# Performance work log

Measured on AMD Instinct MI355X. Metric: run time of the kernel, lower is better.

Reference implementation:

```python
import jax, jax.numpy as jnp
import numpy as np

B, T, I, H, O = 64, 512, 256, 512, 10


def _init(key, shape, fan):
    k = 1.0 / np.sqrt(fan)
    return jax.random.uniform(key, shape, jnp.float32, -k, k)


def setup_inputs() -> dict:
    key = jax.random.key(0)
    ks = jax.random.split(key, 16)
    return {
        "x": jax.random.normal(ks[0], (B, T, I), jnp.float32),
        # LSTM params (PyTorch gate order: i, f, g, o)
        "lstm_w_ih": _init(ks[1], (4 * H, I), H),
        "lstm_w_hh": _init(ks[2], (4 * H, H), H),
        "lstm_b_ih": _init(ks[3], (4 * H,), H),
        "lstm_b_hh": _init(ks[4], (4 * H,), H),
        # GRU params (gate order: r, z, n)
        "gru_w_ih": _init(ks[5], (3 * H, H), H),
        "gru_w_hh": _init(ks[6], (3 * H, H), H),
        "gru_b_ih": _init(ks[7], (3 * H,), H),
        "gru_b_hh": _init(ks[8], (3 * H,), H),
        # RNN-tanh params
        "rnn_w_ih": _init(ks[9], (H, H), H),
        "rnn_w_hh": _init(ks[10], (H, H), H),
        "rnn_b_ih": _init(ks[11], (H,), H),
        "rnn_b_hh": _init(ks[12], (H,), H),
        # FC head
        "fc_w": _init(ks[13], (O, H), H),
        "fc_b": _init(ks[14], (O,), H),
    }


def _lstm(x, w_ih, w_hh, b_ih, b_hh):
    # Precompute input projections for all timesteps: [T, B, 4H]
    xg = (jnp.einsum('bti,gi->btg', x, w_ih) + b_ih + b_hh).transpose(1, 0, 2)
    h0 = jnp.zeros((x.shape[0], w_hh.shape[1]), x.dtype)

    def step(carry, xt):
        h, c = carry
        g = xt + h @ w_hh.T
        i, f, gg, o = jnp.split(g, 4, axis=-1)
        c = jax.nn.sigmoid(f) * c + jax.nn.sigmoid(i) * jnp.tanh(gg)
        h = jax.nn.sigmoid(o) * jnp.tanh(c)
        return (h, c), h

    _, hs = jax.lax.scan(step, (h0, h0), xg)
    return hs.transpose(1, 0, 2)  # [B, T, H]


def _gru(x, w_ih, w_hh, b_ih, b_hh):
    xg = (jnp.einsum('bti,gi->btg', x, w_ih) + b_ih).transpose(1, 0, 2)  # [T,B,3H]
    h0 = jnp.zeros((x.shape[0], w_hh.shape[1]), x.dtype)

    def step(h, xt):
        hg = h @ w_hh.T + b_hh
        xr, xz, xn = jnp.split(xt, 3, axis=-1)
        hr, hz, hn = jnp.split(hg, 3, axis=-1)
        r = jax.nn.sigmoid(xr + hr)
        z = jax.nn.sigmoid(xz + hz)
        n = jnp.tanh(xn + r * hn)
        h = (1.0 - z) * n + z * h
        return h, h

    _, hs = jax.lax.scan(step, h0, xg)
    return hs.transpose(1, 0, 2)


def _rnn_tanh(x, w_ih, w_hh, b_ih, b_hh):
    xg = (jnp.einsum('bti,gi->btg', x, w_ih) + b_ih + b_hh).transpose(1, 0, 2)
    h0 = jnp.zeros((x.shape[0], w_hh.shape[1]), x.dtype)

    def step(h, xt):
        h = jnp.tanh(xt + h @ w_hh.T)
        return h, h

    _, hs = jax.lax.scan(step, h0, xg)
    return hs.transpose(1, 0, 2)


def reference(x, lstm_w_ih, lstm_w_hh, lstm_b_ih, lstm_b_hh,
              gru_w_ih, gru_w_hh, gru_b_ih, gru_b_hh,
              rnn_w_ih, rnn_w_hh, rnn_b_ih, rnn_b_hh,
              fc_w, fc_b):
    h = _lstm(x, lstm_w_ih, lstm_w_hh, lstm_b_ih, lstm_b_hh)
    h = _gru(h, gru_w_ih, gru_w_hh, gru_b_ih, gru_b_hh)
    h = _rnn_tanh(h, rnn_w_ih, rnn_w_hh, rnn_b_ih, rnn_b_hh)
    last = h[:, -1]  # [B, H]
    return last @ fc_w.T + fc_b  # [B, O]
```

## Files before the change

### kernel.cpp

```cpp
#include <hip/hip_runtime.h>
#include <cstdint>

typedef _Float16 f16;
typedef _Float16 f16x8 __attribute__((ext_vector_type(8)));
typedef float f32x4 __attribute__((ext_vector_type(4)));
typedef unsigned u32;
typedef u32 u32x4 __attribute__((ext_vector_type(4)));

#define DI static __device__ __forceinline__

constexpr int T = 512, H = 512, Osz = 10;
constexpr int NWG = 256, NTH = 768;
constexpr int GW = 32;
constexpr int GB = 8;
constexpr int BH = 64 * H;
constexpr size_t XH_OFF = 512 * 1024;
constexpr int XH_GRP = 8 * T * 256;

DI float sigf(float x)   { return 1.f / (1.f + __expf(-x)); }
DI float tanhf_(float x) { return 1.f - 2.f / (__expf(2.f * x) + 1.f); }

DI f16x8 cvt8(const float* p) {
  f16x8 r;
#pragma unroll
  for (int j = 0; j < 8; ++j) r[j] = (f16)p[j];
  return r;
}

DI void pin8(f16x8& v) { asm volatile("" : "+v"(v)); }
DI u32 umin_(u32 a, u32 b) { return a < b ? a : b; }

DI void st16_sc1(void* p, f16 v) {
  asm volatile("global_store_short %0, %1, off sc1" :: "v"(p), "v"(v));
}
DI void st32_sc1(void* p, u32 v) {
  asm volatile("global_store_dword %0, %1, off sc1" :: "v"(p), "v"(v));
}
DI void st128_sc1(void* p, f16x8 v) {
  asm volatile("global_store_dwordx4 %0, %1, off sc1" :: "v"(p), "v"(v));
}
DI void vm_drain() { asm volatile("s_waitcnt vmcnt(0)" ::: "memory"); }

DI void ld2_sc1(const void* p0, const void* p1, f16x8& a, f16x8& b) {
  asm volatile(
    "global_load_dwordx4 %0, %2, off sc1\n\t"
    "global_load_dwordx4 %1, %3, off sc1\n\t"
    "s_waitcnt vmcnt(0)"
    : "=&v"(a), "=&v"(b)
    : "v"(p0), "v"(p1)
    : "memory");
}
DI void ld3_sc1(const void* p0, const void* p1, const void* p2,
                f16x8& a, f16x8& b, f16x8& c) {
  asm volatile(
    "global_load_dwordx4 %0, %3, off sc1\n\t"
    "global_load_dwordx4 %1, %4, off sc1\n\t"
    "global_load_dwordx4 %2, %5, off sc1\n\t"
    "s_waitcnt vmcnt(0)"
    : "=&v"(a), "=&v"(b), "=&v"(c)
    : "v"(p0), "v"(p1), "v"(p2)
    : "memory");
}

DI void ldrow8(const f16* base, f16x8* A) {
  asm volatile(
    "global_load_dwordx4 %0, %8, off sc1\n\t"
    "global_load_dwordx4 %1, %8, off offset:16 sc1\n\t"
    "global_load_dwordx4 %2, %8, off offset:32 sc1\n\t"
    "global_load_dwordx4 %3, %8, off offset:48 sc1\n\t"
    "global_load_dwordx4 %4, %8, off offset:64 sc1\n\t"
    "global_load_dwordx4 %5, %8, off offset:80 sc1\n\t"
    "global_load_dwordx4 %6, %8, off offset:96 sc1\n\t"
    "global_load_dwordx4 %7, %8, off offset:112 sc1\n\t"
    "s_waitcnt vmcnt(0)"
    : "=&v"(A[0]), "=&v"(A[1]), "=&v"(A[2]), "=&v"(A[3]),
      "=&v"(A[4]), "=&v"(A[5]), "=&v"(A[6]), "=&v"(A[7])
    : "v"(base)
    : "memory");
}

DI u32 slots_min(const u32* base) {
  u32x4 a0, a1, a2, a3, a4, a5, a6, a7;
  asm volatile(
    "global_load_dwordx4 %0, %8, off sc1\n\t"
    "global_load_dwordx4 %1, %8, off offset:16 sc1\n\t"
    "global_load_dwordx4 %2, %8, off offset:32 sc1\n\t"
    "global_load_dwordx4 %3, %8, off offset:48 sc1\n\t"
    "global_load_dwordx4 %4, %8, off offset:64 sc1\n\t"
    "global_load_dwordx4 %5, %8, off offset:80 sc1\n\t"
    "global_load_dwordx4 %6, %8, off offset:96 sc1\n\t"
    "global_load_dwordx4 %7, %8, off offset:112 sc1\n\t"
    "s_waitcnt vmcnt(0)"
    : "=&v"(a0), "=&v"(a1), "=&v"(a2), "=&v"(a3),
      "=&v"(a4), "=&v"(a5), "=&v"(a6), "=&v"(a7)
    : "v"(base)
    : "memory");
  u32 m = 0xFFFFFFFFu;
#define MIN4_(v) m = umin_(m, umin_(umin_(v[0], v[1]), umin_(v[2], v[3])))
  MIN4_(a0); MIN4_(a1); MIN4_(a2); MIN4_(a3);
  MIN4_(a4); MIN4_(a5); MIN4_(a6); MIN4_(a7);
#undef MIN4_
  return m;
}

DI void barrier_arrive(u32* slots, int w32, u32 val, int tid) {
  __syncthreads();
  if (tid == 0) st32_sc1(&slots[w32], val);
}
DI void barrier_wait(u32* slots, u32 target, int tid) {
  if (tid == 0) {
    u32 spins = 0;
    while (slots_min(slots) < target) {
      if (++spins > 300000u) break;
    }
  }
  __syncthreads();
}

__global__ __launch_bounds__(NTH, 1) void rnn_all(
    const float* __restrict__ x,
    const float* __restrict__ lwih, const float* __restrict__ lwhh,
    const float* __restrict__ lbih, const float* __restrict__ lbhh,
    const float* __restrict__ gwih, const float* __restrict__ gwhh,
    const float* __restrict__ gbih, const float* __restrict__ gbhh,
    const float* __restrict__ rwih, const float* __restrict__ rwhh,
    const float* __restrict__ rbih, const float* __restrict__ rbhh,
    const float* __restrict__ fcw, const float* __restrict__ fcb,
    float* __restrict__ out, char* __restrict__ ws)
{
  __shared__ __align__(16) u32 HSu[3 * 2048];
  __shared__ __align__(16) u32 XS[1024];
  __shared__ float P[12][16][20];
  __shared__ float sb[16][11];

  const int tid  = threadIdx.x;
  const int bid  = blockIdx.x;
  const int grp  = bid & 7;
  const int w32  = bid >> 3;
  const int bg0  = grp * GB;
  const int col0 = w32 * 16;
  const int w    = tid >> 6;
  const int lane = tid & 63;
  const int ln   = lane & 15;
  const int lk   = lane >> 4;

  u32* slots = reinterpret_cast<u32*>(ws) + (size_t)grp * 64;
  f16* HB = reinterpret_cast<f16*>(ws + 4096);
  f16* xh = reinterpret_cast<f16*>(ws + XH_OFF) + (size_t)grp * XH_GRP;

  f16x8 Bw[24];
#pragma unroll
  for (int ks = 16; ks < 24; ++ks) Bw[ks] = (f16x8)(f16)0.f;
  if (w < 4) {
    const int row = w * 512 + col0 + ln;
    const float* ph  = lwhh + (size_t)row * 512 + lk * 8;
    const float* px2 = lwih + (size_t)row * 256 + lk * 8;
#pragma unroll
    for (int ks = 0; ks < 16; ++ks) Bw[ks] = cvt8(ph + ks * 32);
#pragma unroll
    for (int ks = 0; ks < 8;  ++ks) Bw[16 + ks] = cvt8(px2 + ks * 32);
  } else if (w < 7) {
    const int row = (w - 4) * 512 + col0 + ln;
    const float* p = gwih + (size_t)row * 512 + lk * 8;
#pragma unroll
    for (int ks = 0; ks < 16; ++ks) Bw[ks] = cvt8(p + ks * 32);
  } else if (w < 10) {
    const int row = (w - 7) * 512 + col0 + ln;
    const float* p = gwhh + (size_t)row * 512 + lk * 8;
#pragma unroll
    for (int ks = 0; ks < 16; ++ks) Bw[ks] = cvt8(p + ks * 32);
  } else if (w == 10) {
    const float* p = rwhh + (size_t)(col0 + ln) * 512 + lk * 8;
#pragma unroll
    for (int ks = 0; ks < 16; ++ks) Bw[ks] = cvt8(p + ks * 32);
  } else {
    const float* p = rwih + (size_t)(col0 + ln) * 512 + lk * 8;
#pragma unroll
    for (int ks = 0; ks < 16; ++ks) Bw[ks] = cvt8(p + ks * 32);
  }
#pragma unroll
  for (int ks = 0; ks < 24; ++ks) pin8(Bw[ks]);

  for (int i = tid; i < 16 * 11; i += NTH) {
    int c = i / 11, j = i % 11, col = col0 + c;
    float v;
    if (j < 4)       v = lbih[j * 512 + col] + lbhh[j * 512 + col];
    else if (j < 7)  v = gbih[(j - 4) * 512 + col];
    else if (j < 10) v = gbhh[(j - 7) * 512 + col];
    else             v = rbih[col] + rbhh[col];
    sb[c][j] = v;
  }

  {
    const float* xg_ = x + (size_t)bg0 * (T * 256);
    for (int c = w32 * NTH + tid; c < XH_GRP / 8; c += GW * NTH) {
      const float* p = xg_ + (size_t)c * 8;
      f16x8 v;
#pragma unroll
      for (int j = 0; j < 8; ++j) v[j] = (f16)p[j];
      st128_sc1((void*)(xh + (size_t)c * 8), v);
    }
  }
  {
    int i = w32 * NTH + tid;
    if (i < 12288) {
      int buf = i >> 12, r = i & 4095, par = r >> 11, row = (r >> 8) & 7, cu = r & 255;
      void* p = (void*)(HB + (size_t)buf * 2 * BH + (size_t)par * BH
                           + (size_t)(bg0 + row) * H + cu * 2);
      st32_sc1(p, 0u);
    }
  }
  vm_drain();

  barrier_arrive(slots, w32, 1u, tid);

  float creg = 0.f, hgreg = 0.f;

  const int hbuf = (w < 7) ? 0 : ((w == 10) ? 2 : 1);

#pragma unroll 1
  for (int s = 0; s <= T + 1; ++s) {
    barrier_wait(slots, (u32)(s + 1), tid);

    const int cur = s & 1, prev = cur ^ 1;
    const int sc = (s < T) ? s : (T - 1);

    {
      int s0 = tid, s1 = tid + NTH;
      int b0 = s0 >> 9, r0 = s0 & 511, row0 = r0 >> 6, sr0 = r0 & 63;
      int b1 = s1 >> 9, r1 = s1 & 511, row1 = r1 >> 6, sr1 = r1 & 63;
      const f16* p0 = HB + (size_t)b0 * 2 * BH + (size_t)prev * BH
                         + (size_t)(bg0 + row0) * H + sr0 * 8;
      const f16* p1 = HB + (size_t)b1 * 2 * BH + (size_t)prev * BH
                         + (size_t)(bg0 + row1) * H + sr1 * 8;
      f16x8 va, vb;
      if (w < 4) {
        int xrow = tid >> 5, xsr = tid & 31;
        const f16* p2 = xh + ((size_t)xrow << 17) + (size_t)sc * 256 + xsr * 8;
        f16x8 vc;
        ld3_sc1(p0, p1, p2, va, vb, vc);
        *reinterpret_cast<f16x8*>(
            &XS[(((u32)xrow << 5) | ((u32)(xsr ^ xrow))) << 2]) = vc;
      } else {
        ld2_sc1(p0, p1, va, vb);
      }
      *reinterpret_cast<f16x8*>(&HSu[(b0 << 11) + row0 * 256 + ((sr0 ^ row0) << 2)]) = va;
      *reinterpret_cast<f16x8*>(&HSu[(b1 << 11) + row1 * 256 + ((sr1 ^ row1) << 2)]) = vb;
    }
    __syncthreads();

    const u32 rw_ = (u32)(ln & 7);
    const u32 abase = (u32)hbuf * 2048u + rw_ * 256u;

    f32x4 acc = {0.f, 0.f, 0.f, 0.f};
    if (w < 4) {
#pragma unroll
      for (int ks = 0; ks < 8; ++ks) {
        const f16x8 a = *reinterpret_cast<const f16x8*>(
            &XS[(((rw_ << 5) | (((u32)(ks * 4 + lk)) ^ rw_)) << 2)]);
        acc = __builtin_amdgcn_mfma_f32_16x16x32_f16(a, Bw[16 + ks], acc, 0, 0, 0);
      }
    }
#pragma unroll
    for (int ks = 0; ks < 16; ++ks) {
      const f16x8 a = *reinterpret_cast<const f16x8*>(
          &HSu[abase + ((((u32)(ks * 4 + lk)) ^ rw_) << 2)]);
      acc = __builtin_amdgcn_mfma_f32_16x16x32_f16(a, Bw[ks], acc, 0, 0, 0);
    }

    if (lk < 2)
      *reinterpret_cast<f32x4*>(&P[w][ln][lk * 4]) = acc;
    __syncthreads();

    if (tid < 128) {
      const int cb = tid >> 4, cc = tid & 15;
      const int gb = bg0 + cb, col = col0 + cc;

      float iL = sigf(P[0][cc][cb] + sb[cc][0]);
      float fL = sigf(P[1][cc][cb] + sb[cc][1]);
      float gL = tanhf_(P[2][cc][cb] + sb[cc][2]);
      float oL = sigf(P[3][cc][cb] + sb[cc][3]);
      float cn = fL * creg + iL * gL;
      float hLv = oL * tanhf_(cn);
      float xr = P[4][cc][cb] + sb[cc][4];
      float xz = P[5][cc][cb] + sb[cc][5];
      float xn = P[6][cc][cb] + sb[cc][6];
      float hr = P[7][cc][cb] + sb[cc][7];
      float hz = P[8][cc][cb] + sb[cc][8];
      float hn = P[9][cc][cb] + sb[cc][9];
      float rg = sigf(xr + hr), zg = sigf(xz + hz);
      float ng = tanhf_(xn + rg * hn);
      float hGv = (1.f - zg) * ng + zg * hgreg;
      float hRv = tanhf_(P[10][cc][cb] + P[11][cc][cb] + sb[cc][10]);

      f16* rowp = HB + (size_t)cur * BH + (size_t)gb * H + col;
      if (s < T)            { creg = cn; st16_sc1((void*)rowp, (f16)hLv); }
      if (s >= 1 && s <= T) { hgreg = hGv; st16_sc1((void*)(rowp + 2 * BH), (f16)hGv); }
      if (s >= 2)           st16_sc1((void*)(rowp + 4 * BH), (f16)hRv);
      vm_drain();
    }
    barrier_arrive(slots, w32, (u32)(s + 2), tid);
  }

  if (w32 == 0) {
    barrier_wait(slots, (u32)(T + 3), tid);
    if (tid < 640) {
      const f16* hlast = HB + 4 * BH + BH;
      int bo = tid >> 3, kq = tid & 7;
      int bl = bo / 10, o = bo % 10;
      const f16* ph = hlast + (size_t)(bg0 + bl) * H + kq * 64;
      const float* pw = fcw + (size_t)o * H + kq * 64;
      f16x8 v[8];
      ldrow8(ph, v);
      float a = 0.f;
#pragma unroll
      for (int q = 0; q < 8; ++q)
#pragma unroll
        for (int j = 0; j < 8; ++j) a += (float)v[q][j] * pw[q * 8 + j];
      a += __shfl_xor(a, 1);
      a += __shfl_xor(a, 2);
      a += __shfl_xor(a, 4);
      if (kq == 0) out[(bg0 + bl) * Osz + o] = a + fcb[o];
    }
  }
}

extern "C" void kernel_launch(void* const* d_in, const int* in_sizes, int n_in,
                              void* d_out, int out_size, void* d_ws, size_t ws_size,
                              hipStream_t stream) {
  (void)in_sizes; (void)n_in; (void)out_size; (void)ws_size;
  const float* x    = (const float*)d_in[0];
  const float* lwih = (const float*)d_in[1];
  const float* lwhh = (const float*)d_in[2];
  const float* lbih = (const float*)d_in[3];
  const float* lbhh = (const float*)d_in[4];
  const float* gwih = (const float*)d_in[5];
  const float* gwhh = (const float*)d_in[6];
  const float* gbih = (const float*)d_in[7];
  const float* gbhh = (const float*)d_in[8];
  const float* rwih = (const float*)d_in[9];
  const float* rwhh = (const float*)d_in[10];
  const float* rbih = (const float*)d_in[11];
  const float* rbhh = (const float*)d_in[12];
  const float* fcw  = (const float*)d_in[13];
  const float* fcb  = (const float*)d_in[14];
  float* outp = (float*)d_out;
  char* wsp   = (char*)d_ws;

  hipMemsetAsync(d_ws, 0, 4096, stream);

  rnn_all<<<dim3(NWG), dim3(NTH), 0, stream>>>(
      x, lwih, lwhh, lbih, lbhh, gwih, gwhh, gbih, gbhh,
      rwih, rwhh, rbih, rbhh, fcw, fcb, outp, wsp);
}
```

Measured before the change: 2.075 ms.

## Shrink per-step epilogue to one wave and drop the arrive barrier

The per-timestep gate epilogue now runs on a single 64-lane wave. Each lane computes two adjacent columns and writes them as packed 32-bit stores instead of 16-bit ones. That wave signals its own arrival right after draining its stores, so the block-wide __syncthreads before each arrive is gone. Spin-polling moves to a thread in another wave, and the loop-invariant load and LDS addresses are hoisted out of the step loop. The aim is to cut per-step sync and store latency on the serial critical path, at the cost of more ALU work per epilogue lane.

```diff
diff --git a/kernel.cpp b/kernel.cpp
--- a/kernel.cpp
+++ b/kernel.cpp
@@ -17,6 +17,8 @@
 constexpr size_t XH_OFF = 512 * 1024;
 constexpr int XH_GRP = 8 * T * 256;
 
+union F16x2 { u32 u; f16 h[2]; };
+
 DI float sigf(float x)   { return 1.f / (1.f + __expf(-x)); }
 DI float tanhf_(float x) { return 1.f - 2.f / (__expf(2.f * x) + 1.f); }
 
@@ -30,9 +32,6 @@
 DI void pin8(f16x8& v) { asm volatile("" : "+v"(v)); }
 DI u32 umin_(u32 a, u32 b) { return a < b ? a : b; }
 
-DI void st16_sc1(void* p, f16 v) {
-  asm volatile("global_store_short %0, %1, off sc1" :: "v"(p), "v"(v));
-}
 DI void st32_sc1(void* p, u32 v) {
   asm volatile("global_store_dword %0, %1, off sc1" :: "v"(p), "v"(v));
 }
@@ -103,12 +102,13 @@
   return m;
 }
 
-DI void barrier_arrive(u32* slots, int w32, u32 val, int tid) {
+DI void arrive_full(u32* slots, int w32, u32 val, int tid) {
   __syncthreads();
   if (tid == 0) st32_sc1(&slots[w32], val);
 }
+
 DI void barrier_wait(u32* slots, u32 target, int tid) {
-  if (tid == 0) {
+  if (tid == 704) {
     u32 spins = 0;
     while (slots_min(slots) < target) {
       if (++spins > 300000u) break;
@@ -212,11 +212,19 @@
   }
   vm_drain();
 
-  barrier_arrive(slots, w32, 1u, tid);
-
-  float creg = 0.f, hgreg = 0.f;
+  arrive_full(slots, w32, 1u, tid);
+
+  float creg0 = 0.f, creg1 = 0.f, hgreg0 = 0.f, hgreg1 = 0.f;
 
   const int hbuf = (w < 7) ? 0 : ((w == 10) ? 2 : 1);
+
+  const int s0_ = tid, s1_ = tid + NTH;
+  const int b0_ = s0_ >> 9, r0_ = s0_ & 511, row0_ = r0_ >> 6, sr0_ = r0_ & 63;
+  const int b1_ = s1_ >> 9, r1_ = s1_ & 511, row1_ = r1_ >> 6, sr1_ = r1_ & 63;
+  const f16* pa_base = HB + (size_t)b0_ * 2 * BH + (size_t)(bg0 + row0_) * H + sr0_ * 8;
+  const f16* pb_base = HB + (size_t)b1_ * 2 * BH + (size_t)(bg0 + row1_) * H + sr1_ * 8;
+  const u32 lds_a = (u32)((b0_ << 11) + row0_ * 256 + ((sr0_ ^ row0_) << 2));
+  const u32 lds_b = (u32)((b1_ << 11) + row1_ * 256 + ((sr1_ ^ row1_) << 2));
 
 #pragma unroll 1
   for (int s = 0; s <= T + 1; ++s) {
@@ -226,13 +234,8 @@
     const int sc = (s < T) ? s : (T - 1);
 
     {
-      int s0 = tid, s1 = tid + NTH;
-      int b0 = s0 >> 9, r0 = s0 & 511, row0 = r0 >> 6, sr0 = r0 & 63;
-      int b1 = s1 >> 9, r1 = s1 & 511, row1 = r1 >> 6, sr1 = r1 & 63;
-      const f16* p0 = HB + (size_t)b0 * 2 * BH + (size_t)prev * BH
-                         + (size_t)(bg0 + row0) * H + sr0 * 8;
-      const f16* p1 = HB + (size_t)b1 * 2 * BH + (size_t)prev * BH
-                         + (size_t)(bg0 + row1) * H + sr1 * 8;
+      const f16* p0 = pa_base + (size_t)prev * BH;
+      const f16* p1 = pb_base + (size_t)prev * BH;
       f16x8 va, vb;
       if (w < 4) {
         int xrow = tid >> 5, xsr = tid & 31;
@@ -244,8 +247,8 @@
       } else {
         ld2_sc1(p0, p1, va, vb);
       }
-      *reinterpret_cast<f16x8*>(&HSu[(b0 << 11) + row0 * 256 + ((sr0 ^ row0) << 2)]) = va;
-      *reinterpret_cast<f16x8*>(&HSu[(b1 << 11) + row1 * 256 + ((sr1 ^ row1) << 2)]) = vb;
+      *reinterpret_cast<f16x8*>(&HSu[lds_a]) = va;
+      *reinterpret_cast<f16x8*>(&HSu[lds_b]) = vb;
     }
     __syncthreads();
 
@@ -272,34 +275,46 @@
       *reinterpret_cast<f32x4*>(&P[w][ln][lk * 4]) = acc;
     __syncthreads();
 
-    if (tid < 128) {
-      const int cb = tid >> 4, cc = tid & 15;
-      const int gb = bg0 + cb, col = col0 + cc;
-
-      float iL = sigf(P[0][cc][cb] + sb[cc][0]);
-      float fL = sigf(P[1][cc][cb] + sb[cc][1]);
-      float gL = tanhf_(P[2][cc][cb] + sb[cc][2]);
-      float oL = sigf(P[3][cc][cb] + sb[cc][3]);
-      float cn = fL * creg + iL * gL;
-      float hLv = oL * tanhf_(cn);
-      float xr = P[4][cc][cb] + sb[cc][4];
-      float xz = P[5][cc][cb] + sb[cc][5];
-      float xn = P[6][cc][cb] + sb[cc][6];
-      float hr = P[7][cc][cb] + sb[cc][7];
-      float hz = P[8][cc][cb] + sb[cc][8];
-      float hn = P[9][cc][cb] + sb[cc][9];
-      float rg = sigf(xr + hr), zg = sigf(xz + hz);
-      float ng = tanhf_(xn + rg * hn);
-      float hGv = (1.f - zg) * ng + zg * hgreg;
-      float hRv = tanhf_(P[10][cc][cb] + P[11][cc][cb] + sb[cc][10]);
-
-      f16* rowp = HB + (size_t)cur * BH + (size_t)gb * H + col;
-      if (s < T)            { creg = cn; st16_sc1((void*)rowp, (f16)hLv); }
-      if (s >= 1 && s <= T) { hgreg = hGv; st16_sc1((void*)(rowp + 2 * BH), (f16)hGv); }
-      if (s >= 2)           st16_sc1((void*)(rowp + 4 * BH), (f16)hRv);
+    if (tid < 64) {
+      const int cb = tid >> 3, cp = tid & 7;
+      const int gb = bg0 + cb;
+      const int c0 = 2 * cp;
+
+      F16x2 oL_, oG_, oR_;
+      float cn_[2], hg_[2];
+#pragma unroll
+      for (int c = 0; c < 2; ++c) {
+        const int cc = c0 + c;
+        const float crold = c ? creg1 : creg0;
+        const float hgold = c ? hgreg1 : hgreg0;
+        float iL = sigf(P[0][cc][cb] + sb[cc][0]);
+        float fL = sigf(P[1][cc][cb] + sb[cc][1]);
+        float gL = tanhf_(P[2][cc][cb] + sb[cc][2]);
+        float oL = sigf(P[3][cc][cb] + sb[cc][3]);
+        float cn = fL * crold + iL * gL;
+        float hLv = oL * tanhf_(cn);
+        float xr = P[4][cc][cb] + sb[cc][4];
+        float xz = P[5][cc][cb] + sb[cc][5];
+        float xn = P[6][cc][cb] + sb[cc][6];
+        float hr = P[7][cc][cb] + sb[cc][7];
+        float hz = P[8][cc][cb] + sb[cc][8];
+        float hn = P[9][cc][cb] + sb[cc][9];
+        float rg = sigf(xr + hr), zg = sigf(xz + hz);
+        float ng = tanhf_(xn + rg * hn);
+        float hGv = (1.f - zg) * ng + zg * hgold;
+        float hRv = tanhf_(P[10][cc][cb] + P[11][cc][cb] + sb[cc][10]);
+        cn_[c] = cn; hg_[c] = hGv;
+        oL_.h[c] = (f16)hLv; oG_.h[c] = (f16)hGv; oR_.h[c] = (f16)hRv;
+      }
+      f16* rowp = HB + (size_t)cur * BH + (size_t)gb * H + col0 + c0;
+      if (s < T)            { creg0 = cn_[0]; creg1 = cn_[1];
+                              st32_sc1((void*)rowp, oL_.u); }
+      if (s >= 1 && s <= T) { hgreg0 = hg_[0]; hgreg1 = hg_[1];
+                              st32_sc1((void*)(rowp + 2 * BH), oG_.u); }
+      if (s >= 2)           st32_sc1((void*)(rowp + 4 * BH), oR_.u);
       vm_drain();
-    }
-    barrier_arrive(slots, w32, (u32)(s + 2), tid);
+      if (tid == 0) st32_sc1(&slots[w32], (u32)(s + 2));
+    }
   }
 
   if (w32 == 0) {
```

After: 3.246 ms. +56.4%, slower.
